# Kernel tuning notes

Measured on AMD Instinct MI355X. Metric: run time of the kernel, lower is better.

Reference implementation:

```python
import jax, jax.numpy as jnp
import numpy as np

N_NODES = 50000
N_EDGES = 800000
D = 64
H = 4
ALPHA = 0.2  # LeakyReLU negative slope


def gat_conv(x, W, a_s, a_d, src, dst):
    # x: [N, D], W: [D, D], a_s/a_d: [D]
    h = x @ W                               # [N, D]
    s_src = h @ a_s                         # [N]
    s_dst = h @ a_d                         # [N]
    e = jax.nn.leaky_relu(s_src[src] + s_dst[dst], ALPHA)   # [E]
    # segment softmax over incoming edges of each dst node
    m = jax.ops.segment_max(e, dst, num_segments=N_NODES)   # [N]
    ex = jnp.exp(e - m[dst])                                # [E]
    z = jax.ops.segment_sum(ex, dst, num_segments=N_NODES)  # [N]
    attn = ex / (z[dst] + 1e-16)                            # [E]
    out = jax.ops.segment_sum(h[src] * attn[:, None], dst, num_segments=N_NODES)
    return out


def gat_layer(x, W, a_s, a_d, src, dst):
    # sequential application of H single-head convs (as in the torch code);
    # dropout is identity in eval mode
    out = x
    for i in range(H):
        out = gat_conv(out, W[i], a_s[i], a_d[i], src, dst)
    return jax.nn.elu(out)


def setup_inputs() -> dict:
    key = jax.random.key(0)
    ks = jax.random.split(key, 8)
    sc = 1.0 / np.sqrt(D)
    features = jax.random.normal(ks[0], (N_NODES, D), dtype=jnp.float32)
    edge_index = jax.random.randint(ks[1], (2, N_EDGES), 0, N_NODES, dtype=jnp.int64)
    W1 = jax.random.normal(ks[2], (H, D, D), dtype=jnp.float32) * sc
    a_src1 = jax.random.normal(ks[3], (H, D), dtype=jnp.float32) * sc
    a_dst1 = jax.random.normal(ks[4], (H, D), dtype=jnp.float32) * sc
    W2 = jax.random.normal(ks[5], (H, D, D), dtype=jnp.float32) * sc
    a_src2 = jax.random.normal(ks[6], (H, D), dtype=jnp.float32) * sc
    a_dst2 = jax.random.normal(ks[7], (H, D), dtype=jnp.float32) * sc
    return {"features": features, "edge_index": edge_index,
            "W1": W1, "a_src1": a_src1, "a_dst1": a_dst1,
            "W2": W2, "a_src2": a_src2, "a_dst2": a_dst2}


def reference(features, edge_index, W1, a_src1, a_dst1, W2, a_src2, a_dst2):
    src, dst = edge_index[0], edge_index[1]
    x = gat_layer(features, W1, a_src1, a_dst1, src, dst)
    # F.dropout between layers is identity in eval mode
    x = gat_layer(x, W2, a_src2, a_dst2, src, dst)
    return x
```

## Files before the change

### kernel.cpp

```cpp
#include <hip/hip_runtime.h>
#include <hip/hip_bf16.h>

#define N_NODES 50000
#define N_EDGES 800000
#define DIM 64
#define NB 391
#define NBLK 128
#define CHUNK 6250
#define CAP 4096
#define NTILES 3125
#define FROWS 32
#define FPAD 68

typedef __attribute__((ext_vector_type(8))) short bf16x8;
typedef __attribute__((ext_vector_type(4))) float f32x4;

__device__ __forceinline__ float bf2f(unsigned short u) {
  return __uint_as_float(((unsigned int)u) << 16);
}
__device__ __forceinline__ unsigned short f2bf(float f) {
  unsigned int x = __float_as_uint(f);
  unsigned int r = (x + 0x7fffu + ((x >> 16) & 1u)) >> 16;
  return (unsigned short)r;
}

__global__ void k_detect(const unsigned short* __restrict__ feat,
                         const unsigned int* __restrict__ eidx,
                         int* __restrict__ flags) {
  int lane = threadIdx.x;
  float v = bf2f(feat[2 * lane]);
  bool big = !(fabsf(v) < 1000.0f);
  unsigned long long bb = __ballot(big);
  unsigned int w = eidx[2 * lane + 1];
  unsigned long long bz = __ballot(w == 0u);
  if (lane == 0) {
    flags[0] = (__popcll(bb) < 8) ? 1 : 0;
    flags[1] = (__popcll(bz) == 64) ? 1 : 0;
  }
}

__device__ __forceinline__ int eidx_at(const int* __restrict__ p, int k, int i64) {
  return p[i64 ? (k << 1) : k];
}

__global__ __launch_bounds__(256) void k_wprep(
    const void* __restrict__ W1, const void* __restrict__ A1s,
    const void* __restrict__ A1d, const void* __restrict__ W2,
    const void* __restrict__ A2s, const void* __restrict__ A2d,
    const int* __restrict__ flags, unsigned short* __restrict__ wfH,
    unsigned short* __restrict__ wfL, unsigned short* __restrict__ baf) {
  __shared__ float Wsh[DIM * DIM];
  __shared__ float was[DIM], wad[DIM];
  const int b = blockIdx.x;
  const int t = threadIdx.x;
  const int bf = flags[0];
  const void* Wv = (b < 4) ? W1 : W2;
  const void* av = (b < 4) ? A1s : A2s;
  const void* dv = (b < 4) ? A1d : A2d;
  const int hm = (b < 4) ? b : b - 4;
  for (int i = t; i < DIM * DIM; i += 256)
    Wsh[i] = bf ? bf2f(((const unsigned short*)Wv)[hm * DIM * DIM + i])
                : ((const float*)Wv)[hm * DIM * DIM + i];
  __syncthreads();
  if (t < 128) {
    int k = t & 63, isd = t >> 6;
    const void* aptr = isd ? dv : av;
    float acc = 0.f;
    for (int c = 0; c < DIM; ++c) {
      float a = bf ? bf2f(((const unsigned short*)aptr)[hm * DIM + c])
                   : ((const float*)aptr)[hm * DIM + c];
      acc = fmaf(Wsh[k * DIM + c], a, acc);
    }
    (isd ? wad : was)[k] = acc;
  }
  __syncthreads();
  for (int idx = t; idx < 512; idx += 256) {
    int lane = idx & 63, ks = (idx >> 6) & 1, cb = idx >> 7;
    int g4 = lane >> 4, r16 = lane & 15;
    int fo = (((b * 4 + cb) * 2 + ks) * 64 + lane) * 8;
#pragma unroll
    for (int j = 0; j < 8; ++j) {
      int k = 32 * ks + 8 * g4 + j;
      float w = Wsh[k * DIM + 16 * cb + r16];
      unsigned short hu = f2bf(w);
      wfH[fo + j] = hu;
      wfL[fo + j] = f2bf(w - bf2f(hu));
    }
  }
  for (int idx = t; idx < 128; idx += 256) {
    int lane = idx & 63, ks = idx >> 6;
    int g4 = lane >> 4, r16 = lane & 15;
    int fo = ((b * 2 + ks) * 64 + lane) * 8;
#pragma unroll
    for (int j = 0; j < 8; ++j) {
      int k = 32 * ks + 8 * g4 + j;
      unsigned short u = 0;
      if (r16 < 4) {
        float w_ = (r16 < 2) ? was[k] : wad[k];
        unsigned short uh = f2bf(w_);
        u = (r16 & 1) ? f2bf(w_ - bf2f(uh)) : uh;
      }
      baf[fo + j] = u;
    }
  }
}

__global__ __launch_bounds__(256) void k_split(const void* __restrict__ feat,
                                               const int* __restrict__ flags,
                                               unsigned short* __restrict__ xh,
                                               unsigned short* __restrict__ xl) {
  int i = (blockIdx.x * 256 + threadIdx.x) * 4;
  if (i >= N_NODES * DIM) return;
  if (flags[0]) {
    ushort4 v = *(const ushort4*)((const unsigned short*)feat + i);
    *(ushort4*)(xh + i) = v;
    *(ushort4*)(xl + i) = make_ushort4(0, 0, 0, 0);
  } else {
    float4 f = *(const float4*)((const float*)feat + i);
    ushort4 h4, l4;
    h4.x = f2bf(f.x); l4.x = f2bf(f.x - bf2f(h4.x));
    h4.y = f2bf(f.y); l4.y = f2bf(f.y - bf2f(h4.y));
    h4.z = f2bf(f.z); l4.z = f2bf(f.z - bf2f(h4.z));
    h4.w = f2bf(f.w); l4.w = f2bf(f.w - bf2f(h4.w));
    *(ushort4*)(xh + i) = h4;
    *(ushort4*)(xl + i) = l4;
  }
}

__global__ void k_scan1(const int* __restrict__ in, int* __restrict__ out,
                        int* __restrict__ bsum, int n) {
  __shared__ int sm[256];
  int t = threadIdx.x, b = blockIdx.x, i = b * 256 + t;
  int v = (i < n) ? in[i] : 0;
  sm[t] = v;
  __syncthreads();
  for (int off = 1; off < 256; off <<= 1) {
    int x = (t >= off) ? sm[t - off] : 0;
    __syncthreads();
    sm[t] += x;
    __syncthreads();
  }
  if (i < n) out[i] = sm[t] - v;
  if (t == 255) bsum[b] = sm[t];
}

__global__ void k_scan2(int* __restrict__ bsum, int nb) {
  __shared__ int sm[256];
  int t = threadIdx.x;
  int v = (t < nb) ? bsum[t] : 0;
  sm[t] = v;
  __syncthreads();
  for (int off = 1; off < 256; off <<= 1) {
    int x = (t >= off) ? sm[t - off] : 0;
    __syncthreads();
    sm[t] += x;
    __syncthreads();
  }
  if (t < nb) bsum[t] = sm[t] - v;
}

__global__ void k_scan3(int* __restrict__ out, const int* __restrict__ bsum, int n) {
  int t = threadIdx.x, b = blockIdx.x, i = b * 256 + t;
  if (i < n) out[i] += bsum[b];
}

__global__ __launch_bounds__(256) void k_hist1(const int* __restrict__ eidx,
                                               const int* __restrict__ flags,
                                               int* __restrict__ hist) {
  __shared__ int h[NB];
  int t = threadIdx.x, b = blockIdx.x;
  for (int i = t; i < NB; i += 256) h[i] = 0;
  __syncthreads();
  int i64 = flags[1];
  int lo = b * CHUNK;
  for (int i = t; i < CHUNK; i += 256) {
    int d = eidx_at(eidx, N_EDGES + lo + i, i64);
    atomicAdd(&h[d >> 7], 1);
  }
  __syncthreads();
  for (int i = t; i < NB; i += 256) hist[i * NBLK + b] = h[i];
}

__global__ __launch_bounds__(256) void k_scatter(const int* __restrict__ eidx,
                                                 const int* __restrict__ flags,
                                                 const int* __restrict__ hscan,
                                                 int2* __restrict__ ebuf) {
  __shared__ int cur[NB];
  int t = threadIdx.x, b = blockIdx.x;
  for (int i = t; i < NB; i += 256) cur[i] = hscan[i * NBLK + b];
  __syncthreads();
  int i64 = flags[1];
  int lo = b * CHUNK;
  for (int i = t; i < CHUNK; i += 256) {
    int d = eidx_at(eidx, N_EDGES + lo + i, i64);
    int s = eidx_at(eidx, lo + i, i64);
    int pos = atomicAdd(&cur[d >> 7], 1);
    ebuf[pos] = make_int2(s, d);
  }
}

__global__ __launch_bounds__(256) void k_place(const int2* __restrict__ ebuf,
                                               const int* __restrict__ hscan,
                                               int* __restrict__ rowp,
                                               int* __restrict__ csr) {
  __shared__ int hcnt[128];
  __shared__ int sm[128];
  __shared__ int cur[128];
  __shared__ int lcsr[CAP];
  int t = threadIdx.x, b = blockIdx.x;
  int lo = hscan[b * NBLK];
  int hi = (b + 1 < NB) ? hscan[(b + 1) * NBLK] : N_EDGES;
  if (t < 128) hcnt[t] = 0;
  __syncthreads();
  for (int i = lo + t; i < hi; i += 256) atomicAdd(&hcnt[ebuf[i].y & 127], 1);
  __syncthreads();
  int v = (t < 128) ? hcnt[t] : 0;
  if (t < 128) sm[t] = v;
  __syncthreads();
  for (int off = 1; off < 128; off <<= 1) {
    int x = (t < 128 && t >= off) ? sm[t - off] : 0;
    __syncthreads();
    if (t < 128) sm[t] += x;
    __syncthreads();
  }
  int d0 = b * 128;
  if (t < 128) {
    int excl = sm[t] - v;
    cur[t] = excl;
    int d = d0 + t;
    if (d < N_NODES) rowp[d] = lo + excl;
  }
  if (b == NB - 1 && t == 0) rowp[N_NODES] = N_EDGES;
  __syncthreads();
  int seg_sz = hi - lo;
  if (seg_sz <= CAP) {
    for (int i = lo + t; i < hi; i += 256) {
      int2 pr = ebuf[i];
      int pos = atomicAdd(&cur[pr.y & 127], 1);
      lcsr[pos] = pr.x;
    }
    __syncthreads();
    for (int i = t; i < seg_sz; i += 256) csr[lo + i] = lcsr[i];
  } else {
    for (int i = lo + t; i < hi; i += 256) {
      int2 pr = ebuf[i];
      int pos = atomicAdd(&cur[pr.y & 127], 1);
      csr[lo + pos] = pr.x;
    }
  }
}

__global__ __launch_bounds__(256) void k_gemm(
    const unsigned short* __restrict__ xh, const unsigned short* __restrict__ xl,
    const unsigned short* __restrict__ wfH, const unsigned short* __restrict__ wfL,
    const unsigned short* __restrict__ baf, int mat,
    unsigned short* __restrict__ hb, float* __restrict__ ss,
    float* __restrict__ sd) {
  const int lane = threadIdx.x & 63;
  const int w = blockIdx.x * 4 + (threadIdx.x >> 6);
  const int wtile = w >> 1;
  if (wtile >= NTILES) return;
  const int cbh = (w & 1) * 2;
  const int r16 = lane & 15;
  const int g4 = lane >> 4;
  const int row0 = wtile * 16;

  const bf16x8* WH = (const bf16x8*)wfH;
  const bf16x8* WL = (const bf16x8*)wfL;
  bf16x8 Bh[2][2], Bl[2][2];
#pragma unroll
  for (int c = 0; c < 2; ++c)
#pragma unroll
    for (int ks = 0; ks < 2; ++ks) {
      int fi = ((mat * 4 + cbh + c) * 2 + ks) * 64 + lane;
      Bh[c][ks] = WH[fi];
      Bl[c][ks] = WL[fi];
    }

  bf16x8 Ah[2], Al[2];
#pragma unroll
  for (int ks = 0; ks < 2; ++ks) {
    Ah[ks] = *(const bf16x8*)(xh + (row0 + r16) * DIM + 32 * ks + 8 * g4);
    Al[ks] = *(const bf16x8*)(xl + (row0 + r16) * DIM + 32 * ks + 8 * g4);
  }

  f32x4 acc[2];
#pragma unroll
  for (int c = 0; c < 2; ++c) {
    acc[c] = (f32x4){0.f, 0.f, 0.f, 0.f};
#pragma unroll
    for (int ks = 0; ks < 2; ++ks) {
      acc[c] = __builtin_amdgcn_mfma_f32_16x16x32_bf16(Ah[ks], Bh[c][ks], acc[c], 0, 0, 0);
      acc[c] = __builtin_amdgcn_mfma_f32_16x16x32_bf16(Al[ks], Bh[c][ks], acc[c], 0, 0, 0);
      acc[c] = __builtin_amdgcn_mfma_f32_16x16x32_bf16(Ah[ks], Bl[c][ks], acc[c], 0, 0, 0);
    }
  }

#pragma unroll
  for (int c = 0; c < 2; ++c)
#pragma unroll
    for (int reg = 0; reg < 4; ++reg)
      hb[(row0 + 4 * g4 + reg) * DIM + (cbh + c) * 16 + r16] = f2bf(acc[c][reg]);

  if (cbh == 0) {
    f32x4 acc2 = (f32x4){0.f, 0.f, 0.f, 0.f};
#pragma unroll
    for (int ks = 0; ks < 2; ++ks) {
      bf16x8 Ba = *(const bf16x8*)(baf + ((mat * 2 + ks) * 64 + lane) * 8);
      acc2 = __builtin_amdgcn_mfma_f32_16x16x32_bf16(Ah[ks], Ba, acc2, 0, 0, 0);
      acc2 = __builtin_amdgcn_mfma_f32_16x16x32_bf16(Al[ks], Ba, acc2, 0, 0, 0);
    }
#pragma unroll
    for (int reg = 0; reg < 4; ++reg) {
      float tmp = acc2[reg] + __shfl_xor(acc2[reg], 1);
      int row = row0 + 4 * g4 + reg;
      if (r16 == 0) ss[row] = tmp;
      else if (r16 == 2) sd[row] = tmp;
    }
  }
}

__device__ __forceinline__ void quad_accum(const unsigned short* __restrict__ hb,
                                           const int2* __restrict__ lps, int cl,
                                           int quarter, int c16, float4& acc) {
  const int quads = (cl + 3) >> 2;
#pragma unroll 4
  for (int tt = 0; tt < quads; ++tt) {
    int j = 4 * tt + quarter;
    int2 pv = lps[j];
    float pj = __int_as_float(pv.x);
    int sj = pv.y;
    ushort4 hv = *(const ushort4*)(hb + sj * DIM + 4 * c16);
    acc.x = fmaf(pj, bf2f(hv.x), acc.x);
    acc.y = fmaf(pj, bf2f(hv.y), acc.y);
    acc.z = fmaf(pj, bf2f(hv.z), acc.z);
    acc.w = fmaf(pj, bf2f(hv.w), acc.w);
  }
}

__device__ __forceinline__ void agg_node_big(
    const unsigned short* __restrict__ hb, const float* __restrict__ ss,
    float sdn, int base, int deg, const int* __restrict__ csr, int lane,
    int quarter, int c16, int2* __restrict__ lpw, float4& acc, float& zo) {
  float z = 0.f;
  for (int c = 0; c < deg; c += 64) {
    int j = c + lane;
    float p = 0.f; int s = 0;
    if (j < deg) {
      s = csr[base + j];
      float sc = ss[s] + sdn;
      sc = (sc >= 0.f) ? sc : 0.2f * sc;
      p = __expf(sc);
    }
    lpw[lane] = make_int2(__float_as_int(p), s);
    __builtin_amdgcn_wave_barrier();
    z += p;
    const int cl = (deg - c < 64) ? (deg - c) : 64;
    quad_accum(hb, lpw, cl, quarter, c16, acc);
    __builtin_amdgcn_wave_barrier();
  }
#pragma unroll
  for (int off = 32; off > 0; off >>= 1) z += __shfl_xor(z, off);
  zo = z;
}

__device__ __forceinline__ void agg_core(
    const unsigned short* __restrict__ hb, const float* __restrict__ ss,
    const float* __restrict__ sd, const int* __restrict__ rowp,
    const int* __restrict__ csr, int node, int lane, int quarter, int c16,
    int do_elu, int2* __restrict__ lpw, float& ox, float& oy, float& oz,
    float& ow) {
  const int base = rowp[node];
  const int deg = rowp[node + 1] - base;
  const float sdn = sd[node];
  float4 acc = {0.f, 0.f, 0.f, 0.f};
  float z;
  if (deg <= 64) {
    int s = 0;
    float p = 0.f;
    if (lane < deg) {
      s = csr[base + lane];
      float t = ss[s] + sdn;
      t = (t >= 0.f) ? t : 0.2f * t;
      p = __expf(t);
    }
    lpw[lane] = make_int2(__float_as_int(p), s);
    z = p;
    __builtin_amdgcn_wave_barrier();
    quad_accum(hb, lpw, deg, quarter, c16, acc);
    __builtin_amdgcn_wave_barrier();
#pragma unroll
    for (int off = 32; off > 0; off >>= 1) z += __shfl_xor(z, off);
  } else {
    agg_node_big(hb, ss, sdn, base, deg, csr, lane, quarter, c16, lpw, acc, z);
  }
  acc.x += __shfl_xor(acc.x, 16);
  acc.y += __shfl_xor(acc.y, 16);
  acc.z += __shfl_xor(acc.z, 16);
  acc.w += __shfl_xor(acc.w, 16);
  acc.x += __shfl_xor(acc.x, 32);
  acc.y += __shfl_xor(acc.y, 32);
  acc.z += __shfl_xor(acc.z, 32);
  acc.w += __shfl_xor(acc.w, 32);
  float inv = 1.f / (z + 1e-16f);
  ox = acc.x * inv; oy = acc.y * inv;
  oz = acc.z * inv; ow = acc.w * inv;
  if (do_elu) {
    ox = (ox > 0.f) ? ox : expm1f(ox);
    oy = (oy > 0.f) ? oy : expm1f(oy);
    oz = (oz > 0.f) ? oz : expm1f(oz);
    ow = (ow > 0.f) ? ow : expm1f(ow);
  }
}

__global__ __launch_bounds__(512) void k_fused(
    const unsigned short* __restrict__ hb_in, const float* __restrict__ ss_in,
    const float* __restrict__ sd_in, const int* __restrict__ rowp,
    const int* __restrict__ csr, const unsigned short* __restrict__ wfH,
    const unsigned short* __restrict__ wfL, const unsigned short* __restrict__ baf,
    int mat, int do_elu, unsigned short* __restrict__ hb_out,
    float* __restrict__ ss_out, float* __restrict__ sd_out) {
  __shared__ float outT[FROWS][FPAD];
  __shared__ __align__(16) int2 lps[8][64];
  const int tid = threadIdx.x;
  const int lane = tid & 63;
  const int w = tid >> 6;
  const int quarter = lane >> 4;
  const int c16 = lane & 15;
  const int blk = blockIdx.x;

  for (int j = 0; j < 4; ++j) {
    const int row = w * 4 + j;
    const int node = blk * FROWS + row;
    float ox = 0.f, oy = 0.f, oz = 0.f, ow = 0.f;
    if (node < N_NODES)
      agg_core(hb_in, ss_in, sd_in, rowp, csr, node, lane, quarter, c16,
               do_elu, &lps[w][0], ox, oy, oz, ow);
    if (quarter == 0) {
      float4 o4 = {ox, oy, oz, ow};
      *(float4*)&outT[row][4 * c16] = o4;
    }
  }
  __syncthreads();

  const int t = w >> 2;
  const int cb = w & 3;
  const int r16 = c16;
  const int g4 = quarter;

  bf16x8 Ah[2], Al[2];
#pragma unroll
  for (int ks = 0; ks < 2; ++ks) {
    const float* src = &outT[t * 16 + r16][32 * ks + 8 * g4];
    float4 f0 = *(const float4*)src;
    float4 f1 = *(const float4*)(src + 4);
    float v[8] = {f0.x, f0.y, f0.z, f0.w, f1.x, f1.y, f1.z, f1.w};
#pragma unroll
    for (int jj = 0; jj < 8; ++jj) {
      unsigned short hu = f2bf(v[jj]);
      Ah[ks][jj] = (short)hu;
      Al[ks][jj] = (short)f2bf(v[jj] - bf2f(hu));
    }
  }

  const bf16x8* WH = (const bf16x8*)wfH;
  const bf16x8* WL = (const bf16x8*)wfL;
  f32x4 acc = (f32x4){0.f, 0.f, 0.f, 0.f};
#pragma unroll
  for (int ks = 0; ks < 2; ++ks) {
    int fi = ((mat * 4 + cb) * 2 + ks) * 64 + lane;
    bf16x8 Bh = WH[fi];
    bf16x8 Bl = WL[fi];
    acc = __builtin_amdgcn_mfma_f32_16x16x32_bf16(Ah[ks], Bh, acc, 0, 0, 0);
    acc = __builtin_amdgcn_mfma_f32_16x16x32_bf16(Al[ks], Bh, acc, 0, 0, 0);
    acc = __builtin_amdgcn_mfma_f32_16x16x32_bf16(Ah[ks], Bl, acc, 0, 0, 0);
  }
#pragma unroll
  for (int reg = 0; reg < 4; ++reg) {
    int row = blk * FROWS + t * 16 + 4 * g4 + reg;
    if (row < N_NODES) hb_out[row * DIM + cb * 16 + r16] = f2bf(acc[reg]);
  }

  if (cb == 0) {
    f32x4 acc2 = (f32x4){0.f, 0.f, 0.f, 0.f};
#pragma unroll
    for (int ks = 0; ks < 2; ++ks) {
      bf16x8 Ba = *(const bf16x8*)(baf + ((mat * 2 + ks) * 64 + lane) * 8);
      acc2 = __builtin_amdgcn_mfma_f32_16x16x32_bf16(Ah[ks], Ba, acc2, 0, 0, 0);
      acc2 = __builtin_amdgcn_mfma_f32_16x16x32_bf16(Al[ks], Ba, acc2, 0, 0, 0);
    }
#pragma unroll
    for (int reg = 0; reg < 4; ++reg) {
      float tmp = acc2[reg] + __shfl_xor(acc2[reg], 1);
      int row = blk * FROWS + t * 16 + 4 * g4 + reg;
      if (row < N_NODES) {
        if (r16 == 0) ss_out[row] = tmp;
        else if (r16 == 2) sd_out[row] = tmp;
      }
    }
  }
}

__global__ __launch_bounds__(256) void k_agg(
    const unsigned short* __restrict__ hb, const float* __restrict__ ss,
    const float* __restrict__ sd, const int* __restrict__ rowp,
    const int* __restrict__ csr, void* __restrict__ out_final,
    const int* __restrict__ flags, int do_elu) {
  __shared__ __align__(16) int2 lps[4][64];
  const int lane = threadIdx.x & 63;
  const int quarter = lane >> 4;
  const int c16 = lane & 15;
  const int w = threadIdx.x >> 6;
  const int node = blockIdx.x * 4 + w;
  float ox, oy, oz, ow;
  agg_core(hb, ss, sd, rowp, csr, node, lane, quarter, c16, do_elu,
           &lps[w][0], ox, oy, oz, ow);
  if (quarter == 0) {
    int idx = node * DIM + 4 * c16;
    if (flags[0]) {
      ushort4 o4 = {f2bf(ox), f2bf(oy), f2bf(oz), f2bf(ow)};
      *(ushort4*)((unsigned short*)out_final + idx) = o4;
    } else {
      float4 o4 = {ox, oy, oz, ow};
      *(float4*)((float*)out_final + idx) = o4;
    }
  }
}

extern "C" void kernel_launch(void* const* d_in, const int* in_sizes, int n_in,
                              void* d_out, int out_size, void* d_ws, size_t ws_size,
                              hipStream_t stream) {
  const void* feat = d_in[0];
  const int* eidx = (const int*)d_in[1];

  unsigned short* xh1 = (unsigned short*)d_ws;
  unsigned short* xl1 = xh1 + N_NODES * DIM;
  unsigned short* hbA = xl1 + N_NODES * DIM;
  unsigned short* hbB = hbA + N_NODES * DIM;
  unsigned short* wfH = hbB + N_NODES * DIM;
  unsigned short* wfL = wfH + 32768;
  unsigned short* baf = wfL + 32768;
  int2* ebuf = (int2*)(baf + 8192);
  float* ssA = (float*)(ebuf + N_EDGES);
  float* sdA = ssA + N_NODES;
  float* ssB = sdA + N_NODES;
  float* sdB = ssB + N_NODES;
  int* csr  = (int*)(sdB + N_NODES);
  int* hist = csr + N_EDGES;
  int* hscan = hist + NB * NBLK;
  int* bsum = hscan + NB * NBLK;
  int* rowp = bsum + 256;
  int* flags = rowp + N_NODES + 1;

  const int NH = NB * NBLK;
  const int SBH = (NH + 255) / 256;

  k_detect<<<1, 64, 0, stream>>>((const unsigned short*)feat,
                                 (const unsigned int*)eidx, flags);
  k_wprep<<<8, 256, 0, stream>>>(d_in[2], d_in[3], d_in[4],
                                 d_in[5], d_in[6], d_in[7],
                                 flags, wfH, wfL, baf);
  k_split<<<(N_NODES * DIM / 4 + 255) / 256, 256, 0, stream>>>(feat, flags, xh1, xl1);
  k_hist1<<<NBLK, 256, 0, stream>>>(eidx, flags, hist);
  k_scan1<<<SBH, 256, 0, stream>>>(hist, hscan, bsum, NH);
  k_scan2<<<1, 256, 0, stream>>>(bsum, SBH);
  k_scan3<<<SBH, 256, 0, stream>>>(hscan, bsum, NH);
  k_scatter<<<NBLK, 256, 0, stream>>>(eidx, flags, hscan, ebuf);
  k_place<<<NB, 256, 0, stream>>>(ebuf, hscan, rowp, csr);

  const int GB = (2 * NTILES + 3) / 4;
  const int FB = (N_NODES + FROWS - 1) / FROWS;

  k_gemm<<<GB, 256, 0, stream>>>(xh1, xl1, wfH, wfL, baf, 0, hbA, ssA, sdA);

  for (int k = 0; k < 7; ++k) {
    const unsigned short* hin = (k & 1) ? hbB : hbA;
    const float* sin_ = (k & 1) ? ssB : ssA;
    const float* din = (k & 1) ? sdB : sdA;
    unsigned short* hout = (k & 1) ? hbA : hbB;
    float* sout = (k & 1) ? ssA : ssB;
    float* dout = (k & 1) ? sdA : sdB;
    k_fused<<<FB, 512, 0, stream>>>(hin, sin_, din, rowp, csr, wfH, wfL, baf,
                                    k + 1, (k == 3) ? 1 : 0, hout, sout, dout);
  }

  k_agg<<<N_NODES / 4, 256, 0, stream>>>(hbB, ssB, sdB, rowp, csr, d_out,
                                         flags, 1);
}
```

Before: 363.8 us.

## Fuse feature bf16 split into first GEMM and batch low-degree node aggregation

Removes the separate k_split kernel and its hi/lo scratch buffers. The first GEMM now reads the raw features and splits fp32 into bf16 hi/lo in registers, skipping the Al MFMAs when the input is already bf16. In k_fused, each wave handles its four nodes together when every degree is at most 64. It loads CSR entries, scores and exponentials for all four at once, without max subtraction, before the gather-accumulate, to expose more memory-level parallelism. Dropping the max subtraction could overflow exp for large scores, and the shared lps array grows fourfold.

```diff
diff --git a/kernel.cpp b/kernel.cpp
--- a/kernel.cpp
+++ b/kernel.cpp
@@ -105,28 +105,6 @@
   }
 }
 
-__global__ __launch_bounds__(256) void k_split(const void* __restrict__ feat,
-                                               const int* __restrict__ flags,
-                                               unsigned short* __restrict__ xh,
-                                               unsigned short* __restrict__ xl) {
-  int i = (blockIdx.x * 256 + threadIdx.x) * 4;
-  if (i >= N_NODES * DIM) return;
-  if (flags[0]) {
-    ushort4 v = *(const ushort4*)((const unsigned short*)feat + i);
-    *(ushort4*)(xh + i) = v;
-    *(ushort4*)(xl + i) = make_ushort4(0, 0, 0, 0);
-  } else {
-    float4 f = *(const float4*)((const float*)feat + i);
-    ushort4 h4, l4;
-    h4.x = f2bf(f.x); l4.x = f2bf(f.x - bf2f(h4.x));
-    h4.y = f2bf(f.y); l4.y = f2bf(f.y - bf2f(h4.y));
-    h4.z = f2bf(f.z); l4.z = f2bf(f.z - bf2f(h4.z));
-    h4.w = f2bf(f.w); l4.w = f2bf(f.w - bf2f(h4.w));
-    *(ushort4*)(xh + i) = h4;
-    *(ushort4*)(xl + i) = l4;
-  }
-}
-
 __global__ void k_scan1(const int* __restrict__ in, int* __restrict__ out,
                         int* __restrict__ bsum, int n) {
   __shared__ int sm[256];
@@ -251,11 +229,12 @@
 }
 
 __global__ __launch_bounds__(256) void k_gemm(
-    const unsigned short* __restrict__ xh, const unsigned short* __restrict__ xl,
+    const void* __restrict__ xv,
     const unsigned short* __restrict__ wfH, const unsigned short* __restrict__ wfL,
     const unsigned short* __restrict__ baf, int mat,
-    unsigned short* __restrict__ hb, float* __restrict__ ss,
-    float* __restrict__ sd) {
+    const int* __restrict__ flags, unsigned short* __restrict__ hb,
+    float* __restrict__ ss, float* __restrict__ sd) {
+  const int bf = flags[0];
   const int lane = threadIdx.x & 63;
   const int w = blockIdx.x * 4 + (threadIdx.x >> 6);
   const int wtile = w >> 1;
@@ -278,10 +257,24 @@
     }
 
   bf16x8 Ah[2], Al[2];
-#pragma unroll
-  for (int ks = 0; ks < 2; ++ks) {
-    Ah[ks] = *(const bf16x8*)(xh + (row0 + r16) * DIM + 32 * ks + 8 * g4);
-    Al[ks] = *(const bf16x8*)(xl + (row0 + r16) * DIM + 32 * ks + 8 * g4);
+  if (bf) {
+    const unsigned short* xp = (const unsigned short*)xv + (row0 + r16) * DIM + 8 * g4;
+#pragma unroll
+    for (int ks = 0; ks < 2; ++ks) Ah[ks] = *(const bf16x8*)(xp + 32 * ks);
+  } else {
+    const float* xp = (const float*)xv + (row0 + r16) * DIM + 8 * g4;
+#pragma unroll
+    for (int ks = 0; ks < 2; ++ks) {
+      float4 f0 = *(const float4*)(xp + 32 * ks);
+      float4 f1 = *(const float4*)(xp + 32 * ks + 4);
+      float v[8] = {f0.x, f0.y, f0.z, f0.w, f1.x, f1.y, f1.z, f1.w};
+#pragma unroll
+      for (int j = 0; j < 8; ++j) {
+        unsigned short hu = f2bf(v[j]);
+        Ah[ks][j] = (short)hu;
+        Al[ks][j] = (short)f2bf(v[j] - bf2f(hu));
+      }
+    }
   }
 
   f32x4 acc[2];
@@ -291,7 +284,8 @@
 #pragma unroll
     for (int ks = 0; ks < 2; ++ks) {
       acc[c] = __builtin_amdgcn_mfma_f32_16x16x32_bf16(Ah[ks], Bh[c][ks], acc[c], 0, 0, 0);
-      acc[c] = __builtin_amdgcn_mfma_f32_16x16x32_bf16(Al[ks], Bh[c][ks], acc[c], 0, 0, 0);
+      if (!bf)
+        acc[c] = __builtin_amdgcn_mfma_f32_16x16x32_bf16(Al[ks], Bh[c][ks], acc[c], 0, 0, 0);
       acc[c] = __builtin_amdgcn_mfma_f32_16x16x32_bf16(Ah[ks], Bl[c][ks], acc[c], 0, 0, 0);
     }
   }
@@ -308,7 +302,8 @@
     for (int ks = 0; ks < 2; ++ks) {
       bf16x8 Ba = *(const bf16x8*)(baf + ((mat * 2 + ks) * 64 + lane) * 8);
       acc2 = __builtin_amdgcn_mfma_f32_16x16x32_bf16(Ah[ks], Ba, acc2, 0, 0, 0);
-      acc2 = __builtin_amdgcn_mfma_f32_16x16x32_bf16(Al[ks], Ba, acc2, 0, 0, 0);
+      if (!bf)
+        acc2 = __builtin_amdgcn_mfma_f32_16x16x32_bf16(Al[ks], Ba, acc2, 0, 0, 0);
     }
 #pragma unroll
     for (int reg = 0; reg < 4; ++reg) {
@@ -421,24 +416,93 @@
     int mat, int do_elu, unsigned short* __restrict__ hb_out,
     float* __restrict__ ss_out, float* __restrict__ sd_out) {
   __shared__ float outT[FROWS][FPAD];
-  __shared__ __align__(16) int2 lps[8][64];
+  __shared__ __align__(16) int2 lps[8][4][64];
   const int tid = threadIdx.x;
   const int lane = tid & 63;
   const int w = tid >> 6;
   const int quarter = lane >> 4;
   const int c16 = lane & 15;
   const int blk = blockIdx.x;
-
+  const int node0 = blk * FROWS + w * 4;
+
+  int bp[5];
+#pragma unroll
+  for (int j = 0; j < 5; ++j) {
+    int idx = node0 + j;
+    bp[j] = rowp[(idx < N_NODES) ? idx : N_NODES];
+  }
+  int deg[4];
+  float sdn[4];
+#pragma unroll
   for (int j = 0; j < 4; ++j) {
-    const int row = w * 4 + j;
-    const int node = blk * FROWS + row;
-    float ox = 0.f, oy = 0.f, oz = 0.f, ow = 0.f;
-    if (node < N_NODES)
-      agg_core(hb_in, ss_in, sd_in, rowp, csr, node, lane, quarter, c16,
-               do_elu, &lps[w][0], ox, oy, oz, ow);
-    if (quarter == 0) {
-      float4 o4 = {ox, oy, oz, ow};
-      *(float4*)&outT[row][4 * c16] = o4;
+    deg[j] = bp[j + 1] - bp[j];
+    int idx = node0 + j;
+    sdn[j] = sd_in[(idx < N_NODES) ? idx : (N_NODES - 1)];
+  }
+
+  if (deg[0] <= 64 && deg[1] <= 64 && deg[2] <= 64 && deg[3] <= 64) {
+    int s4[4];
+    float p4[4];
+#pragma unroll
+    for (int j = 0; j < 4; ++j)
+      s4[j] = (lane < deg[j]) ? csr[bp[j] + lane] : 0;
+#pragma unroll
+    for (int j = 0; j < 4; ++j) {
+      float t = ss_in[s4[j]] + sdn[j];
+      t = (t >= 0.f) ? t : 0.2f * t;
+      p4[j] = (lane < deg[j]) ? __expf(t) : 0.f;
+    }
+#pragma unroll
+    for (int j = 0; j < 4; ++j)
+      lps[w][j][lane] = make_int2(__float_as_int(p4[j]), s4[j]);
+    __builtin_amdgcn_wave_barrier();
+
+    float4 acc[4];
+#pragma unroll
+    for (int j = 0; j < 4; ++j) acc[j] = (float4){0.f, 0.f, 0.f, 0.f};
+#pragma unroll
+    for (int j = 0; j < 4; ++j)
+      quad_accum(hb_in, &lps[w][j][0], deg[j], quarter, c16, acc[j]);
+
+#pragma unroll
+    for (int j = 0; j < 4; ++j) {
+      float z = p4[j];
+#pragma unroll
+      for (int off = 32; off > 0; off >>= 1) z += __shfl_xor(z, off);
+      float4 a = acc[j];
+      a.x += __shfl_xor(a.x, 16);
+      a.y += __shfl_xor(a.y, 16);
+      a.z += __shfl_xor(a.z, 16);
+      a.w += __shfl_xor(a.w, 16);
+      a.x += __shfl_xor(a.x, 32);
+      a.y += __shfl_xor(a.y, 32);
+      a.z += __shfl_xor(a.z, 32);
+      a.w += __shfl_xor(a.w, 32);
+      float inv = 1.f / (z + 1e-16f);
+      float ox = a.x * inv, oy = a.y * inv, oz = a.z * inv, ow = a.w * inv;
+      if (do_elu) {
+        ox = (ox > 0.f) ? ox : expm1f(ox);
+        oy = (oy > 0.f) ? oy : expm1f(oy);
+        oz = (oz > 0.f) ? oz : expm1f(oz);
+        ow = (ow > 0.f) ? ow : expm1f(ow);
+      }
+      if (quarter == 0) {
+        float4 o4 = {ox, oy, oz, ow};
+        *(float4*)&outT[w * 4 + j][4 * c16] = o4;
+      }
+    }
+  } else {
+    for (int j = 0; j < 4; ++j) {
+      const int row = w * 4 + j;
+      const int node = node0 + j;
+      float ox = 0.f, oy = 0.f, oz = 0.f, ow = 0.f;
+      if (node < N_NODES)
+        agg_core(hb_in, ss_in, sd_in, rowp, csr, node, lane, quarter, c16,
+                 do_elu, &lps[w][j][0], ox, oy, oz, ow);
+      if (quarter == 0) {
+        float4 o4 = {ox, oy, oz, ow};
+        *(float4*)&outT[row][4 * c16] = o4;
+      }
     }
   }
   __syncthreads();
@@ -465,33 +529,33 @@
 
   const bf16x8* WH = (const bf16x8*)wfH;
   const bf16x8* WL = (const bf16x8*)wfL;
-  f32x4 acc = (f32x4){0.f, 0.f, 0.f, 0.f};
+  f32x4 acc2 = (f32x4){0.f, 0.f, 0.f, 0.f};
 #pragma unroll
   for (int ks = 0; ks < 2; ++ks) {
     int fi = ((mat * 4 + cb) * 2 + ks) * 64 + lane;
     bf16x8 Bh = WH[fi];
     bf16x8 Bl = WL[fi];
-    acc = __builtin_amdgcn_mfma_f32_16x16x32_bf16(Ah[ks], Bh, acc, 0, 0, 0);
-    acc = __builtin_amdgcn_mfma_f32_16x16x32_bf16(Al[ks], Bh, acc, 0, 0, 0);
-    acc = __builtin_amdgcn_mfma_f32_16x16x32_bf16(Ah[ks], Bl, acc, 0, 0, 0);
+    acc2 = __builtin_amdgcn_mfma_f32_16x16x32_bf16(Ah[ks], Bh, acc2, 0, 0, 0);
+    acc2 = __builtin_amdgcn_mfma_f32_16x16x32_bf16(Al[ks], Bh, acc2, 0, 0, 0);
+    acc2 = __builtin_amdgcn_mfma_f32_16x16x32_bf16(Ah[ks], Bl, acc2, 0, 0, 0);
   }
 #pragma unroll
   for (int reg = 0; reg < 4; ++reg) {
     int row = blk * FROWS + t * 16 + 4 * g4 + reg;
-    if (row < N_NODES) hb_out[row * DIM + cb * 16 + r16] = f2bf(acc[reg]);
+    if (row < N_NODES) hb_out[row * DIM + cb * 16 + r16] = f2bf(acc2[reg]);
   }
 
   if (cb == 0) {
-    f32x4 acc2 = (f32x4){0.f, 0.f, 0.f, 0.f};
+    f32x4 accs = (f32x4){0.f, 0.f, 0.f, 0.f};
 #pragma unroll
     for (int ks = 0; ks < 2; ++ks) {
       bf16x8 Ba = *(const bf16x8*)(baf + ((mat * 2 + ks) * 64 + lane) * 8);
-      acc2 = __builtin_amdgcn_mfma_f32_16x16x32_bf16(Ah[ks], Ba, acc2, 0, 0, 0);
-      acc2 = __builtin_amdgcn_mfma_f32_16x16x32_bf16(Al[ks], Ba, acc2, 0, 0, 0);
+      accs = __builtin_amdgcn_mfma_f32_16x16x32_bf16(Ah[ks], Ba, accs, 0, 0, 0);
+      accs = __builtin_amdgcn_mfma_f32_16x16x32_bf16(Al[ks], Ba, accs, 0, 0, 0);
     }
 #pragma unroll
     for (int reg = 0; reg < 4; ++reg) {
-      float tmp = acc2[reg] + __shfl_xor(acc2[reg], 1);
+      float tmp = accs[reg] + __shfl_xor(accs[reg], 1);
       int row = blk * FROWS + t * 16 + 4 * g4 + reg;
       if (row < N_NODES) {
         if (r16 == 0) ss_out[row] = tmp;
@@ -533,9 +597,7 @@
   const void* feat = d_in[0];
   const int* eidx = (const int*)d_in[1];
 
-  unsigned short* xh1 = (unsigned short*)d_ws;
-  unsigned short* xl1 = xh1 + N_NODES * DIM;
-  unsigned short* hbA = xl1 + N_NODES * DIM;
+  unsigned short* hbA = (unsigned short*)d_ws;
   unsigned short* hbB = hbA + N_NODES * DIM;
   unsigned short* wfH = hbB + N_NODES * DIM;
   unsigned short* wfL = wfH + 32768;
@@ -560,7 +622,6 @@
   k_wprep<<<8, 256, 0, stream>>>(d_in[2], d_in[3], d_in[4],
                                  d_in[5], d_in[6], d_in[7],
                                  flags, wfH, wfL, baf);
-  k_split<<<(N_NODES * DIM / 4 + 255) / 256, 256, 0, stream>>>(feat, flags, xh1, xl1);
   k_hist1<<<NBLK, 256, 0, stream>>>(eidx, flags, hist);
   k_scan1<<<SBH, 256, 0, stream>>>(hist, hscan, bsum, NH);
   k_scan2<<<1, 256, 0, stream>>>(bsum, SBH);
@@ -571,7 +632,7 @@
   const int GB = (2 * NTILES + 3) / 4;
   const int FB = (N_NODES + FROWS - 1) / FROWS;
 
-  k_gemm<<<GB, 256, 0, stream>>>(xh1, xl1, wfH, wfL, baf, 0, hbA, ssA, sdA);
+  k_gemm<<<GB, 256, 0, stream>>>(feat, wfH, wfL, baf, 0, flags, hbA, ssA, sdA);
 
   for (int k = 0; k < 7; ++k) {
     const unsigned short* hin = (k & 1) ? hbB : hbA;
```

Result: faster. 348.5 us (median of 2 runs) (-4.2%).
